# Performance work log

Hardware: AMD Instinct MI355X
Metric: run time of the kernel (lower is better)

The kernel has to match this reference:

```python
import jax, jax.numpy as jnp
import numpy as np

EMBED_SIZE = 512
SCALE = EMBED_SIZE ** 0.5  # note: sqrt(embed_size), not sqrt(head_dim), per source


def setup_inputs() -> dict:
    key = jax.random.key(0)
    kq, kk, kv = jax.random.split(key, 3)
    B, H, S, D = 4, 8, 2048, 64
    query = jax.random.normal(kq, (B, H, S, D), dtype=jnp.float32)
    key_t = jax.random.normal(kk, (B, H, S, D), dtype=jnp.float32)
    value = jax.random.normal(kv, (B, S, H, D), dtype=jnp.float32)  # [b, kv_len, h, d]
    return {"query": query, "key": key_t, "value": value}


def reference(query, key, value):
    # scores: [b, h, q, k]
    scores = jnp.einsum('bhqf,bhkf->bhqk', query, key)
    weight = jax.nn.softmax(scores / SCALE, axis=3)
    # value is [b, l, h, d]; output [b, q, h, d]
    out = jnp.einsum('bhql,blhd->bqhd', weight, value)
    return out
```

## Files before the change

kernel.cpp:

```cpp
#include <hip/hip_runtime.h>
#include <stdint.h>

#define NB 4
#define NH 8
#define NS 2048
#define ND 64
#define BQ 128
#define TK 64
#define KP 72
#define NITG 16

typedef __bf16  bf16x8 __attribute__((ext_vector_type(8)));
typedef float   f32x16 __attribute__((ext_vector_type(16)));
typedef float   f32x4  __attribute__((ext_vector_type(4)));

__device__ __forceinline__ uint32_t pkbf(float x, float y) {
  uint32_t ax = __builtin_bit_cast(uint32_t, x) + 0x8000u;
  uint32_t ay = __builtin_bit_cast(uint32_t, y) + 0x8000u;
  return __builtin_amdgcn_perm(ay, ax, 0x07060302u);
}
__device__ __forceinline__ unsigned short bfu(float x) {
  return (unsigned short)((__builtin_bit_cast(uint32_t, x) + 0x8000u) >> 16);
}

__global__ __launch_bounds__(512, 4) void fa_fwd(
    const float* __restrict__ Q, const float* __restrict__ K,
    const float* __restrict__ V, float* __restrict__ O)
{
  __shared__ __attribute__((aligned(16))) unsigned short smem[2*TK*KP + 2*ND*KP];

  const int tid = threadIdx.x;
  const int wid = tid >> 6, lane = tid & 63;
  const int g   = wid >> 2;
  const int s   = wid & 3;
  const int l31 = lane & 31, h = lane >> 5;
  const int bh = blockIdx.y, b = bh>>3, hh = bh&7;
  const int q0 = blockIdx.x * BQ;
  const int kvbase = g * (NS/2);

  unsigned short* Kl = smem + (size_t)g*TK*KP;
  unsigned short* Vt = smem + 2*TK*KP + (size_t)g*ND*KP;

  const float* Qb = Q + ((size_t)bh*NS + q0)*ND;
  const float* Kb = K + (size_t)bh*NS*ND;
  const float* Vb = V + ((size_t)b*NS*NH + hh)*ND;
  float*       Ob = O + ((size_t)b*NS*NH + hh)*ND;

  const float kSc = 1.44269504088896340736f / 22.6274169979695207808f;

  bf16x8 qf[4];
  {
    const float* qp = Qb + (size_t)(s*32 + l31)*ND + 8*h;
#pragma unroll
    for (int k=0;k<4;++k){
      float4 a = *(const float4*)(qp + 16*k);
      float4 c = *(const float4*)(qp + 16*k + 4);
      uint4 u = make_uint4(pkbf(a.x*kSc,a.y*kSc), pkbf(a.z*kSc,a.w*kSc),
                           pkbf(c.x*kSc,c.y*kSc), pkbf(c.z*kSc,c.w*kSc));
      qf[k] = __builtin_bit_cast(bf16x8, u);
    }
  }

  const int t256  = tid & 255;
  const int krow0 = t256 >> 3, koct = t256 & 7;
  float4 kst[2][2], vst[4];
  auto load_tile = [&](int kt){
    const int kb = kvbase + kt*TK;
#pragma unroll
    for (int i=0;i<2;++i){
      const float* kp = Kb + (size_t)(kb + krow0 + 32*i)*ND + koct*8;
      kst[i][0] = *(const float4*)kp;
      kst[i][1] = *(const float4*)(kp+4);
    }
#pragma unroll
    for (int i=0;i<4;++i)
      vst[i] = *(const float4*)(Vb + (size_t)(kb + lane)*(NH*ND) + (s+4*i)*4);
  };
  auto store_tile = [&](){
#pragma unroll
    for (int i=0;i<2;++i){
      uint4 w = make_uint4(pkbf(kst[i][0].x,kst[i][0].y), pkbf(kst[i][0].z,kst[i][0].w),
                           pkbf(kst[i][1].x,kst[i][1].y), pkbf(kst[i][1].z,kst[i][1].w));
      *(uint4*)&Kl[(size_t)(krow0+32*i)*KP + koct*8] = w;
    }
#pragma unroll
    for (int i=0;i<4;++i){
      int d0 = (s+4*i)*4;
      Vt[(size_t)(d0+0)*KP + lane] = bfu(vst[i].x);
      Vt[(size_t)(d0+1)*KP + lane] = bfu(vst[i].y);
      Vt[(size_t)(d0+2)*KP + lane] = bfu(vst[i].z);
      Vt[(size_t)(d0+3)*KP + lane] = bfu(vst[i].w);
    }
  };

  load_tile(0);
  store_tile();
  __syncthreads();

  const f32x16 zero = {0,0,0,0,0,0,0,0,0,0,0,0,0,0,0,0};
  f32x16 acc[2] = {zero, zero};
  f32x4  l4 = {0.f,0.f,0.f,0.f};

  for (int kt=0; kt<NITG; ++kt){
    load_tile((kt+1) & (NITG-1));

    f32x16 st[2];
#pragma unroll
    for (int t=0;t<2;++t){
      st[t] = zero;
#pragma unroll
      for (int k=0;k<4;++k){
        bf16x8 kf = *(const bf16x8*)&Kl[(size_t)(32*t+l31)*KP + 16*k + 8*h];
        st[t] = __builtin_amdgcn_mfma_f32_32x32x16_bf16(kf, qf[k], st[t], 0,0,0);
      }
    }

    uint32_t P0[2][4], P1[2][4];
#pragma unroll
    for (int t=0;t<2;++t)
#pragma unroll
      for (int u=0;u<4;++u){
        float p0 = __builtin_amdgcn_exp2f(st[t][4*u+0]);
        float p1 = __builtin_amdgcn_exp2f(st[t][4*u+1]);
        float p2 = __builtin_amdgcn_exp2f(st[t][4*u+2]);
        float p3 = __builtin_amdgcn_exp2f(st[t][4*u+3]);
        l4[0]+=p0; l4[1]+=p1; l4[2]+=p2; l4[3]+=p3;
        P0[t][u] = pkbf(p0,p1);
        P1[t][u] = pkbf(p2,p3);
      }

    uint32_t X0[2][2], X1[2][2];
#pragma unroll
    for (int t=0;t<2;++t)
#pragma unroll
      for (int m=0;m<2;++m){
        uint32_t y0 = h ? P0[t][2*m] : P0[t][2*m+1];
        uint32_t y1 = h ? P1[t][2*m] : P1[t][2*m+1];
        X0[t][m] = (uint32_t)__shfl_xor((int)y0, 32, 64);
        X1[t][m] = (uint32_t)__shfl_xor((int)y1, 32, 64);
      }
    bf16x8 pf[4];
#pragma unroll
    for (int k=0;k<4;++k){
      int t = k>>1, m = k&1;
      uint32_t lo0 = h ? X0[t][m]     : P0[t][2*m];
      uint32_t lo1 = h ? X1[t][m]     : P1[t][2*m];
      uint32_t hi0 = h ? P0[t][2*m+1] : X0[t][m];
      uint32_t hi1 = h ? P1[t][2*m+1] : X1[t][m];
      uint4 u = make_uint4(lo0, lo1, hi0, hi1);
      pf[k] = __builtin_bit_cast(bf16x8, u);
    }

#pragma unroll
    for (int gg=0;gg<2;++gg)
#pragma unroll
      for (int k=0;k<4;++k){
        bf16x8 vf = *(const bf16x8*)&Vt[(size_t)(32*gg+l31)*KP + 16*k + 8*h];
        acc[gg] = __builtin_amdgcn_mfma_f32_32x32x16_bf16(vf, pf[k], acc[gg], 0,0,0);
      }

    __syncthreads();
    store_tile();
    __syncthreads();
  }

  float lsum = (l4[0]+l4[1]) + (l4[2]+l4[3]);
  lsum += __shfl_xor(lsum, 32, 64);

  float* C = (float*)smem;
  const int LSOFF = 4*64*33;
  if (g == 1) {
    float* cw = C + (size_t)(s*64 + lane)*33;
#pragma unroll
    for (int gg=0; gg<2; ++gg)
#pragma unroll
      for (int e=0; e<16; ++e) cw[gg*16+e] = acc[gg][e];
    C[LSOFF + s*64 + lane] = lsum;
  }
  __syncthreads();
  if (g == 0) {
    const float* cr = C + (size_t)(s*64 + lane)*33;
#pragma unroll
    for (int gg=0; gg<2; ++gg)
#pragma unroll
      for (int e=0; e<16; ++e) acc[gg][e] += cr[gg*16+e];
    lsum += C[LSOFF + s*64 + lane];

    const float inv = 1.0f / lsum;
    const int q = q0 + s*32 + l31;
    float* op = Ob + (size_t)q*(NH*ND);
#pragma unroll
    for (int gg=0; gg<2; ++gg)
#pragma unroll
      for (int u=0; u<4; ++u){
        float4 o;
        o.x = acc[gg][4*u+0]*inv;
        o.y = acc[gg][4*u+1]*inv;
        o.z = acc[gg][4*u+2]*inv;
        o.w = acc[gg][4*u+3]*inv;
        *(float4*)(op + 32*gg + 8*u + 4*h) = o;
      }
  }
}

extern "C" void kernel_launch(void* const* d_in, const int* in_sizes, int n_in,
                              void* d_out, int out_size, void* d_ws, size_t ws_size,
                              hipStream_t stream) {
  const float* Q = (const float*)d_in[0];
  const float* K = (const float*)d_in[1];
  const float* V = (const float*)d_in[2];
  float* O = (float*)d_out;
  dim3 grid(NS / BQ, NB * NH);
  hipLaunchKernelGGL(fa_fwd, grid, dim3(512), 0, stream, Q, K, V, O);
}
```

Measured before the change: 152.6 us.

## Double-buffer K/V tiles in LDS with one barrier per iteration

Gives each KV group two LDS buffers for its K and transposed V tiles. Each iteration now waits on a single barrier, loads all K and V fragments into registers up front, writes the next tile into the other buffer, and prefetches the tile two steps ahead. This removes one of the two barriers per iteration and lets the LDS stores overlap the MFMA work. In exchange, LDS use doubles and register pressure rises, so launch bounds drop to 2 blocks per CU, which lowers occupancy.

```diff
diff --git a/kernel.cpp b/kernel.cpp
--- a/kernel.cpp
+++ b/kernel.cpp
@@ -23,11 +23,11 @@
   return (unsigned short)((__builtin_bit_cast(uint32_t, x) + 0x8000u) >> 16);
 }
 
-__global__ __launch_bounds__(512, 4) void fa_fwd(
+__global__ __launch_bounds__(512, 2) void fa_fwd(
     const float* __restrict__ Q, const float* __restrict__ K,
     const float* __restrict__ V, float* __restrict__ O)
 {
-  __shared__ __attribute__((aligned(16))) unsigned short smem[2*TK*KP + 2*ND*KP];
+  __shared__ __attribute__((aligned(16))) unsigned short smem[4*TK*KP + 4*ND*KP];
 
   const int tid = threadIdx.x;
   const int wid = tid >> 6, lane = tid & 63;
@@ -38,8 +38,8 @@
   const int q0 = blockIdx.x * BQ;
   const int kvbase = g * (NS/2);
 
-  unsigned short* Kl = smem + (size_t)g*TK*KP;
-  unsigned short* Vt = smem + 2*TK*KP + (size_t)g*ND*KP;
+  unsigned short* Klg = smem + (size_t)g*(2*TK*KP);
+  unsigned short* Vtg = smem + 4*TK*KP + (size_t)g*(2*ND*KP);
 
   const float* Qb = Q + ((size_t)bh*NS + q0)*ND;
   const float* Kb = K + (size_t)bh*NS*ND;
@@ -76,7 +76,9 @@
     for (int i=0;i<4;++i)
       vst[i] = *(const float4*)(Vb + (size_t)(kb + lane)*(NH*ND) + (s+4*i)*4);
   };
-  auto store_tile = [&](){
+  auto store_tile = [&](int bu){
+    unsigned short* Kl = Klg + (size_t)bu*TK*KP;
+    unsigned short* Vt = Vtg + (size_t)bu*ND*KP;
 #pragma unroll
     for (int i=0;i<2;++i){
       uint4 w = make_uint4(pkbf(kst[i][0].x,kst[i][0].y), pkbf(kst[i][0].z,kst[i][0].w),
@@ -94,25 +96,38 @@
   };
 
   load_tile(0);
-  store_tile();
-  __syncthreads();
+  store_tile(0);
+  load_tile(1);
 
   const f32x16 zero = {0,0,0,0,0,0,0,0,0,0,0,0,0,0,0,0};
   f32x16 acc[2] = {zero, zero};
   f32x4  l4 = {0.f,0.f,0.f,0.f};
 
   for (int kt=0; kt<NITG; ++kt){
-    load_tile((kt+1) & (NITG-1));
+    const int cb = kt & 1, nb = cb ^ 1;
+    __syncthreads();
+
+    const unsigned short* Kl = Klg + (size_t)cb*TK*KP;
+    const unsigned short* Vt = Vtg + (size_t)cb*ND*KP;
+    bf16x8 kf[2][4], vf[2][4];
+#pragma unroll
+    for (int t=0;t<2;++t)
+#pragma unroll
+      for (int k=0;k<4;++k){
+        kf[t][k] = *(const bf16x8*)&Kl[(size_t)(32*t+l31)*KP + 16*k + 8*h];
+        vf[t][k] = *(const bf16x8*)&Vt[(size_t)(32*t+l31)*KP + 16*k + 8*h];
+      }
+
+    store_tile(nb);
+    load_tile((kt+2) & (NITG-1));
 
     f32x16 st[2];
 #pragma unroll
     for (int t=0;t<2;++t){
       st[t] = zero;
 #pragma unroll
-      for (int k=0;k<4;++k){
-        bf16x8 kf = *(const bf16x8*)&Kl[(size_t)(32*t+l31)*KP + 16*k + 8*h];
-        st[t] = __builtin_amdgcn_mfma_f32_32x32x16_bf16(kf, qf[k], st[t], 0,0,0);
-      }
+      for (int k=0;k<4;++k)
+        st[t] = __builtin_amdgcn_mfma_f32_32x32x16_bf16(kf[t][k], qf[k], st[t], 0,0,0);
     }
 
     uint32_t P0[2][4], P1[2][4];
@@ -154,19 +169,14 @@
 #pragma unroll
     for (int gg=0;gg<2;++gg)
 #pragma unroll
-      for (int k=0;k<4;++k){
-        bf16x8 vf = *(const bf16x8*)&Vt[(size_t)(32*gg+l31)*KP + 16*k + 8*h];
-        acc[gg] = __builtin_amdgcn_mfma_f32_32x32x16_bf16(vf, pf[k], acc[gg], 0,0,0);
-      }
-
-    __syncthreads();
-    store_tile();
-    __syncthreads();
+      for (int k=0;k<4;++k)
+        acc[gg] = __builtin_amdgcn_mfma_f32_32x32x16_bf16(vf[gg][k], pf[k], acc[gg], 0,0,0);
   }
 
   float lsum = (l4[0]+l4[1]) + (l4[2]+l4[3]);
   lsum += __shfl_xor(lsum, 32, 64);
 
+  __syncthreads();
   float* C = (float*)smem;
   const int LSOFF = 4*64*33;
   if (g == 1) {
```

After: 161.5 us. 5.8% more time.
